# Performance work log

Measured on AMD Instinct MI355X. Metric: run time of the kernel, lower is better.

## Reference

```python
import jax, jax.numpy as jnp
import numpy as np

B, D, T = 8, 1024, 512
HID, NH, NL = 256, 4, 2
OUT = HID // NH  # 64 per-head dim
ALPHA = 0.2      # leaky relu slope
EPS = 1e-5       # layernorm eps


def setup_inputs() -> dict:
    key = jax.random.key(0)
    ks = jax.random.split(key, 10)
    X_obs = jax.random.normal(ks[0], (B, D, T), dtype=jnp.float32)
    mask = (jax.random.uniform(ks[1], (B, D, T)) < 0.8).astype(jnp.float32)
    W_in = jax.random.normal(ks[2], (2 * T, HID), dtype=jnp.float32) * (1.0 / np.sqrt(2 * T))
    b_in = jnp.zeros((HID,), dtype=jnp.float32)
    gat_W = jax.random.normal(ks[3], (NL, NH, HID, OUT), dtype=jnp.float32) * (1.0 / np.sqrt(HID))
    gat_a = jax.random.normal(ks[4], (NL, NH, 2 * OUT), dtype=jnp.float32) * 0.1
    ln_g = jnp.ones((NL, HID), dtype=jnp.float32)
    ln_b = jnp.zeros((NL, HID), dtype=jnp.float32)
    W_out = jax.random.normal(ks[5], (HID, T), dtype=jnp.float32) * (1.0 / np.sqrt(HID))
    b_out = jnp.zeros((T,), dtype=jnp.float32)
    return dict(X_obs=X_obs, mask=mask, W_in=W_in, b_in=b_in, gat_W=gat_W,
                gat_a=gat_a, ln_g=ln_g, ln_b=ln_b, W_out=W_out, b_out=b_out)


def _layer_norm(x, g, b):
    mu = jnp.mean(x, axis=-1, keepdims=True)
    var = jnp.mean((x - mu) ** 2, axis=-1, keepdims=True)
    return (x - mu) * jax.lax.rsqrt(var + EPS) * g + b


def _gat_forward(X_obs, mask, W_in, b_in, gat_W, gat_a, ln_g, ln_b, W_out, b_out):
    # mean-impute per (d, t) position across batch
    obs_sum = jnp.sum(X_obs * mask, axis=0, keepdims=True)
    obs_cnt = jnp.sum(mask, axis=0, keepdims=True)
    pos_mean = obs_sum / (obs_cnt + 1e-10)
    X_mean = X_obs * mask + (1.0 - mask) * pos_mean

    x = jnp.concatenate([X_mean, mask], axis=-1)       # (B, D, 2T)
    h = x @ W_in + b_in                                 # (B, N, HID)

    for l in range(NL):
        Wl = gat_W[l]                                   # (H, HID, OUT)
        a_left = gat_a[l, :, :OUT]                      # (H, OUT)
        a_right = gat_a[l, :, OUT:]                     # (H, OUT)
        hW = jnp.einsum('bnd,hde->bhne', h, Wl)         # (B, H, N, OUT)
        # e_ij = leakyrelu(a_left . h_i + a_right . h_j) -- avoids O(N^2 * 2d) concat
        s_l = jnp.einsum('bhne,he->bhn', hW, a_left)
        s_r = jnp.einsum('bhne,he->bhn', hW, a_right)
        e = jax.nn.leaky_relu(s_l[..., :, None] + s_r[..., None, :], ALPHA)  # (B,H,N,N)
        attn = jax.nn.softmax(e, axis=-1)
        head_out = jnp.einsum('bhnm,bhme->bhne', attn, hW)                   # (B,H,N,OUT)
        h_new = jnp.transpose(head_out, (0, 2, 1, 3)).reshape(h.shape[0], h.shape[1], HID)
        h = _layer_norm(h + h_new, ln_g[l], ln_b[l])

    return h @ W_out + b_out                            # (B, D, T)


def reference(X_obs, mask, W_in, b_in, gat_W, gat_a, ln_g, ln_b, W_out, b_out):
    return _gat_forward(X_obs, mask, W_in, b_in, gat_W, gat_a, ln_g, ln_b, W_out, b_out)
```

## Files before the change

kernel.cpp:

```cpp
#include <hip/hip_runtime.h>
#include <hip/hip_bf16.h>

constexpr int B_   = 8;
constexpr int D_   = 1024;
constexpr int T_   = 512;
constexpr int HID_ = 256;
constexpr int NH_  = 4;
constexpr int NL_  = 2;
constexpr int OUT_ = 64;
constexpr float ALPHA_ = 0.2f;
constexpr float EPS_   = 1e-5f;
constexpr int M_ = B_ * D_;
constexpr int DT_ = D_ * T_;
constexpr int KIN_ = 2 * T_;

typedef __attribute__((ext_vector_type(8))) short short8;
typedef __attribute__((ext_vector_type(4))) float floatx4;

__device__ __forceinline__ unsigned short f2bf(float f) {
    unsigned int u = __float_as_uint(f);
    unsigned int r = u + 0x7fffu + ((u >> 16) & 1u);
    return (unsigned short)(r >> 16);
}
__device__ __forceinline__ float bf2f(unsigned short u) {
    return __uint_as_float((unsigned int)u << 16);
}
__device__ __forceinline__ unsigned int kenc(float f) {
    unsigned int u = __float_as_uint(f);
    return (u & 0x80000000u) ? ~u : (u | 0x80000000u);
}
__device__ __forceinline__ float kdec(unsigned int k) {
    unsigned int u = (k & 0x80000000u) ? (k ^ 0x80000000u) : ~k;
    return __uint_as_float(u);
}

__global__ __launch_bounds__(256) void impute_k(const float* __restrict__ X,
                                                const float* __restrict__ Mk,
                                                unsigned short* __restrict__ Ain) {
    int idx4 = (blockIdx.x * 256 + threadIdx.x) * 4;
    int t = idx4 & (T_ - 1);
    int d = idx4 >> 9;
    float4 x[B_], m[B_];
    float4 s = {0, 0, 0, 0}, c = {0, 0, 0, 0};
#pragma unroll
    for (int b = 0; b < B_; b++) {
        x[b] = *(const float4*)&X[(size_t)b * DT_ + idx4];
        m[b] = *(const float4*)&Mk[(size_t)b * DT_ + idx4];
        s.x += x[b].x * m[b].x; s.y += x[b].y * m[b].y;
        s.z += x[b].z * m[b].z; s.w += x[b].w * m[b].w;
        c.x += m[b].x; c.y += m[b].y; c.z += m[b].z; c.w += m[b].w;
    }
    float4 pm;
    pm.x = s.x / (c.x + 1e-10f); pm.y = s.y / (c.y + 1e-10f);
    pm.z = s.z / (c.z + 1e-10f); pm.w = s.w / (c.w + 1e-10f);
#pragma unroll
    for (int b = 0; b < B_; b++) {
        size_t row = (size_t)b * D_ + d;
        ushort4 xm, mk;
        xm.x = f2bf(x[b].x * m[b].x + (1.f - m[b].x) * pm.x);
        xm.y = f2bf(x[b].y * m[b].y + (1.f - m[b].y) * pm.y);
        xm.z = f2bf(x[b].z * m[b].z + (1.f - m[b].z) * pm.z);
        xm.w = f2bf(x[b].w * m[b].w + (1.f - m[b].w) * pm.w);
        mk.x = f2bf(m[b].x); mk.y = f2bf(m[b].y);
        mk.z = f2bf(m[b].z); mk.w = f2bf(m[b].w);
        *(ushort4*)&Ain[row * KIN_ + t]      = xm;
        *(ushort4*)&Ain[row * KIN_ + T_ + t] = mk;
    }
}

__global__ __launch_bounds__(256) void wprep_k(const float* __restrict__ W_in,
                                               const float* __restrict__ gatW,
                                               const float* __restrict__ W_out,
                                               unsigned short* __restrict__ Wt_in,
                                               unsigned short* __restrict__ Wcat,
                                               unsigned short* __restrict__ WtO,
                                               unsigned int* __restrict__ rmaxkey) {
    int idx = blockIdx.x * 256 + threadIdx.x;
    if (idx < 64) rmaxkey[idx] = 0u;
    if (idx < 262144) {
        int n = idx >> 10, k = idx & 1023;
        Wt_in[idx] = f2bf(W_in[(size_t)k * HID_ + n]);
    } else if (idx < 393216) {
        int j = idx - 262144;
        int l = j >> 16, n = (j >> 8) & 255, k = j & 255;
        int h = n >> 6, e = n & 63;
        Wcat[j] = f2bf(gatW[(((size_t)(l * NH_ + h) * HID_) + k) * OUT_ + e]);
    } else {
        int j = idx - 393216;
        int n = j >> 8, k = j & 255;
        WtO[j] = f2bf(W_out[(size_t)k * T_ + n]);
    }
}

template <int MODE>
__global__ __launch_bounds__(256) void gemm_bf16_k(
        const unsigned short* __restrict__ A,
        const unsigned short* __restrict__ Bt,
        const float* __restrict__ bias,
        float* __restrict__ C,
        unsigned short* __restrict__ Cb,
        const float* __restrict__ ga,
        float* __restrict__ s_l,
        float* __restrict__ s_r,
        unsigned int* __restrict__ rmaxkey,
        int Nsz, int Ksz) {
    __shared__ __align__(16) unsigned short As[2][128 * 32];
    __shared__ __align__(16) unsigned short Bs[2][64 * 32];
    int tid = threadIdx.x;
    int wave = tid >> 6, lane = tid & 63;
    int q = lane >> 4, r16 = lane & 15;
    int rowbase = blockIdx.y * 128;
    int colbase = blockIdx.x * 64;

    int arow0 = tid >> 2,        aoff0 = (tid & 3) * 8;
    int arow1 = (tid + 256) >> 2, aoff1 = (tid & 3) * 8;
    int brow = tid >> 2, boff = (tid & 3) * 8;
    const unsigned short* Ap0 = A + (size_t)(rowbase + arow0) * Ksz + aoff0;
    const unsigned short* Ap1 = A + (size_t)(rowbase + arow1) * Ksz + aoff1;
    const unsigned short* Bp  = Bt + (size_t)(colbase + brow) * Ksz + boff;

    floatx4 acc[2][4];
#pragma unroll
    for (int i = 0; i < 2; i++)
#pragma unroll
        for (int j = 0; j < 4; j++) acc[i][j] = (floatx4)0.f;

    uint4 ar0 = *(const uint4*)Ap0;
    uint4 ar1 = *(const uint4*)Ap1;
    uint4 br  = *(const uint4*)Bp;
    *(uint4*)&As[0][tid * 8]         = ar0;
    *(uint4*)&As[0][(tid + 256) * 8] = ar1;
    *(uint4*)&Bs[0][tid * 8]         = br;

    int nk = Ksz >> 5;
    for (int it = 0; it < nk; it++) {
        int cur = it & 1;
        __syncthreads();
        if (it + 1 < nk) {
            int kt2 = (it + 1) << 5;
            ar0 = *(const uint4*)(Ap0 + kt2);
            ar1 = *(const uint4*)(Ap1 + kt2);
            br  = *(const uint4*)(Bp + kt2);
        }
        short8 a[2], b[4];
#pragma unroll
        for (int mi = 0; mi < 2; mi++)
            a[mi] = *(const short8*)&As[cur][(wave * 32 + mi * 16 + r16) * 32 + q * 8];
#pragma unroll
        for (int ni = 0; ni < 4; ni++)
            b[ni] = *(const short8*)&Bs[cur][(ni * 16 + r16) * 32 + q * 8];
#pragma unroll
        for (int mi = 0; mi < 2; mi++)
#pragma unroll
            for (int ni = 0; ni < 4; ni++)
                acc[mi][ni] = __builtin_amdgcn_mfma_f32_16x16x32_bf16(
                    a[mi], b[ni], acc[mi][ni], 0, 0, 0);
        if (it + 1 < nk) {
            int nxt = cur ^ 1;
            *(uint4*)&As[nxt][tid * 8]         = ar0;
            *(uint4*)&As[nxt][(tid + 256) * 8] = ar1;
            *(uint4*)&Bs[nxt][tid * 8]         = br;
        }
    }
    if constexpr (MODE == 2) {
        int bhh = ((rowbase >> 10) << 2) + blockIdx.x;
        int nbase = (rowbase & (D_ - 1)) + wave * 32;
#pragma unroll
        for (int mi = 0; mi < 2; mi++) {
#pragma unroll
            for (int ni = 0; ni < 4; ni++) {
                int e = ni * 16 + r16;
                ushort4 pk;
                pk.x = f2bf(acc[mi][ni][0]);
                pk.y = f2bf(acc[mi][ni][1]);
                pk.z = f2bf(acc[mi][ni][2]);
                pk.w = f2bf(acc[mi][ni][3]);
                *(ushort4*)&Cb[((size_t)(bhh * 64 + e) << 10) + nbase + mi * 16 + q * 4] = pk;
            }
        }
        const float* gab = ga + blockIdx.x * 2 * OUT_;
        float al4[4], ar4[4];
#pragma unroll
        for (int ni = 0; ni < 4; ni++) {
            al4[ni] = gab[ni * 16 + r16];
            ar4[ni] = gab[OUT_ + ni * 16 + r16];
        }
        float slv[2][4], srv[2][4];
#pragma unroll
        for (int mi = 0; mi < 2; mi++)
#pragma unroll
            for (int rr = 0; rr < 4; rr++) {
                float s1 = 0.f, s2 = 0.f;
#pragma unroll
                for (int ni = 0; ni < 4; ni++) {
                    s1 += acc[mi][ni][rr] * al4[ni];
                    s2 += acc[mi][ni][rr] * ar4[ni];
                }
                slv[mi][rr] = s1;
                srv[mi][rr] = s2;
            }
#pragma unroll
        for (int off = 1; off < 16; off <<= 1) {
#pragma unroll
            for (int mi = 0; mi < 2; mi++)
#pragma unroll
                for (int rr = 0; rr < 4; rr++) {
                    slv[mi][rr] += __shfl_xor(slv[mi][rr], off, 64);
                    srv[mi][rr] += __shfl_xor(srv[mi][rr], off, 64);
                }
        }
        {
            int slot = r16 & 7;
            int mi = slot >> 2, rr = slot & 3;
            int n = nbase + mi * 16 + q * 4 + rr;
            if (r16 < 8) s_l[bhh * D_ + n] = slv[mi][rr];
            else         s_r[bhh * D_ + n] = srv[mi][rr];
        }
        float mx = -1e30f;
#pragma unroll
        for (int mi = 0; mi < 2; mi++)
#pragma unroll
            for (int rr = 0; rr < 4; rr++) mx = fmaxf(mx, srv[mi][rr]);
        if (lane == 0) atomicMax(&rmaxkey[bhh], kenc(mx));
    } else {
#pragma unroll
        for (int mi = 0; mi < 2; mi++) {
#pragma unroll
            for (int rr = 0; rr < 4; rr++) {
                int row = rowbase + wave * 32 + mi * 16 + q * 4 + rr;
#pragma unroll
                for (int ni = 0; ni < 4; ni++) {
                    int col = colbase + ni * 16 + r16;
                    float v = acc[mi][ni][rr] + (bias ? bias[col] : 0.f);
                    C[(size_t)row * Nsz + col] = v;
                    if constexpr (MODE == 1) Cb[(size_t)row * Nsz + col] = f2bf(v);
                }
            }
        }
    }
}

__global__ __launch_bounds__(256) void attn_k(const unsigned short* __restrict__ hwT,
                                              const float* __restrict__ sl_g,
                                              const float* __restrict__ sr_g,
                                              const unsigned int* __restrict__ rmaxkey,
                                              float* __restrict__ hnew) {
    int bh = blockIdx.x;
    int b = bh >> 2, h = bh & 3;
    int tid = threadIdx.x;
    int wave = tid >> 6, lane = tid & 63;
    int q = lane >> 4, r16 = lane & 15;

    __shared__ float srs[D_];
    __shared__ __align__(16) unsigned short Vt[64][136];
    __shared__ float den_lds[64];

    *(float4*)&srs[tid * 4] = *(const float4*)&sr_g[bh * D_ + tid * 4];

    float rm = kdec(rmaxkey[bh]);
    int row0 = blockIdx.y * 64 + wave * 16;
    float sl = sl_g[bh * D_ + row0 + r16];
    float xm = sl + rm;
    float Mn = fmaxf(xm, ALPHA_ * xm);

    floatx4 acc[4];
#pragma unroll
    for (int i = 0; i < 4; i++) acc[i] = (floatx4)0.f;
    float dsum = 0.f;

    const unsigned short* vbase = hwT + ((size_t)(bh * 64) << 10);

    for (int mc = 0; mc < D_; mc += 128) {
        __syncthreads();
#pragma unroll
        for (int i = 0; i < 4; i++) {
            int s = tid + i * 256;
            int e = s >> 4, part = s & 15;
            *(uint4*)&Vt[e][part * 8] = *(const uint4*)&vbase[((size_t)e << 10) + mc + part * 8];
        }
        __syncthreads();
#pragma unroll
        for (int kk = 0; kk < 128; kk += 32) {
            int m0 = mc + kk + q * 8;
            float4 s0 = *(const float4*)&srs[m0];
            float4 s1 = *(const float4*)&srs[m0 + 4];
            float sr8[8] = {s0.x, s0.y, s0.z, s0.w, s1.x, s1.y, s1.z, s1.w};
            float p[8];
#pragma unroll
            for (int j = 0; j < 8; j++) {
                float x = sl + sr8[j];
                float e = fmaxf(x, ALPHA_ * x);
                float pj = __expf(e - Mn);
                dsum += pj;
                p[j] = pj;
            }
            union { unsigned int u[4]; short8 s8; } cv;
#pragma unroll
            for (int j = 0; j < 4; j++) {
                unsigned int lo = (__float_as_uint(p[2 * j]) + 0x8000u) >> 16;
                unsigned int hi = (__float_as_uint(p[2 * j + 1]) + 0x8000u) & 0xffff0000u;
                cv.u[j] = hi | lo;
            }
#pragma unroll
            for (int ni = 0; ni < 4; ni++) {
                short8 bfr = *(const short8*)&Vt[ni * 16 + r16][kk + q * 8];
                acc[ni] = __builtin_amdgcn_mfma_f32_16x16x32_bf16(cv.s8, bfr, acc[ni], 0, 0, 0);
            }
        }
    }
    dsum += __shfl_xor(dsum, 16);
    dsum += __shfl_xor(dsum, 32);
    if (q == 0) den_lds[wave * 16 + r16] = dsum;
    __syncthreads();
#pragma unroll
    for (int rr = 0; rr < 4; rr++) {
        int rloc = q * 4 + rr;
        float rden = 1.f / den_lds[wave * 16 + rloc];
        size_t grow = (size_t)(b * D_ + blockIdx.y * 64 + wave * 16 + rloc);
#pragma unroll
        for (int ni = 0; ni < 4; ni++) {
            hnew[grow * HID_ + h * OUT_ + ni * 16 + r16] = acc[ni][rr] * rden;
        }
    }
}

__global__ __launch_bounds__(256) void addln_k(float* __restrict__ h,
                                               const float* __restrict__ hn,
                                               const float* __restrict__ g,
                                               const float* __restrict__ bb,
                                               unsigned short* __restrict__ hbf) {
    int wave = threadIdx.x >> 6, lane = threadIdx.x & 63;
    size_t row = (size_t)blockIdx.x * 4 + wave;
    float4 a = *(const float4*)&h[row * HID_ + lane * 4];
    float4 r = *(const float4*)&hn[row * HID_ + lane * 4];
    float4 v = {a.x + r.x, a.y + r.y, a.z + r.z, a.w + r.w};
    float s = v.x + v.y + v.z + v.w;
#pragma unroll
    for (int off = 1; off < 64; off <<= 1) s += __shfl_xor(s, off, 64);
    float mu = s * (1.f / HID_);
    float4 d = {v.x - mu, v.y - mu, v.z - mu, v.w - mu};
    float s2 = d.x * d.x + d.y * d.y + d.z * d.z + d.w * d.w;
#pragma unroll
    for (int off = 1; off < 64; off <<= 1) s2 += __shfl_xor(s2, off, 64);
    float rs = rsqrtf(s2 * (1.f / HID_) + EPS_);
    float4 gg = *(const float4*)&g[lane * 4];
    float4 bbv = *(const float4*)&bb[lane * 4];
    float4 res;
    res.x = d.x * rs * gg.x + bbv.x;
    res.y = d.y * rs * gg.y + bbv.y;
    res.z = d.z * rs * gg.z + bbv.z;
    res.w = d.w * rs * gg.w + bbv.w;
    *(float4*)&h[row * HID_ + lane * 4] = res;
    ushort4 pk = {f2bf(res.x), f2bf(res.y), f2bf(res.z), f2bf(res.w)};
    *(ushort4*)&hbf[row * HID_ + lane * 4] = pk;
}

extern "C" void kernel_launch(void* const* d_in, const int* in_sizes, int n_in,
                              void* d_out, int out_size, void* d_ws, size_t ws_size,
                              hipStream_t stream) {
    const float* X_obs = (const float*)d_in[0];
    const float* mask  = (const float*)d_in[1];
    const float* W_in  = (const float*)d_in[2];
    const float* b_in  = (const float*)d_in[3];
    const float* gat_W = (const float*)d_in[4];
    const float* gat_a = (const float*)d_in[5];
    const float* ln_g  = (const float*)d_in[6];
    const float* ln_b  = (const float*)d_in[7];
    const float* W_out = (const float*)d_in[8];
    const float* b_out = (const float*)d_in[9];
    float* out = (float*)d_out;

    char* base = (char*)d_ws;
    unsigned short* Ain  = (unsigned short*)base;
    unsigned short* hwT  = (unsigned short*)base;
    float* hnew = (float*)(base + (4u << 20));
    float* hbuf = (float*)(base + (16u << 20));
    unsigned short* hbf   = (unsigned short*)(base + (24u << 20));
    unsigned short* Wt_in = (unsigned short*)(base + (28u << 20));
    unsigned short* Wcat  = Wt_in + (size_t)HID_ * KIN_;
    unsigned short* WtO   = Wcat + (size_t)NL_ * HID_ * HID_;
    float* slb = (float*)(WtO + (size_t)T_ * HID_);
    float* srb = slb + B_ * NH_ * D_;
    unsigned int* rmaxkey = (unsigned int*)(srb + B_ * NH_ * D_);

    impute_k<<<DT_ / 1024, 256, 0, stream>>>(X_obs, mask, Ain);
    wprep_k<<<2048, 256, 0, stream>>>(W_in, gat_W, W_out, Wt_in, Wcat, WtO, rmaxkey);

    gemm_bf16_k<1><<<dim3(HID_ / 64, M_ / 128), 256, 0, stream>>>(
        Ain, Wt_in, b_in, hbuf, hbf, nullptr, nullptr, nullptr, nullptr,
        HID_, KIN_);

    for (int l = 0; l < NL_; l++) {
        gemm_bf16_k<2><<<dim3(HID_ / 64, M_ / 128), 256, 0, stream>>>(
            hbf, Wcat + (size_t)l * HID_ * HID_, nullptr, nullptr, hwT,
            gat_a + (size_t)l * NH_ * 2 * OUT_, slb, srb, rmaxkey + l * 32,
            HID_, HID_);
        attn_k<<<dim3(B_ * NH_, D_ / 64), 256, 0, stream>>>(
            hwT, slb, srb, rmaxkey + l * 32, hnew);
        addln_k<<<M_ / 4, 256, 0, stream>>>(hbuf, hnew, ln_g + (size_t)l * HID_,
                                            ln_b + (size_t)l * HID_, hbf);
    }

    gemm_bf16_k<0><<<dim3(T_ / 64, M_ / 128), 256, 0, stream>>>(
        hbf, WtO, b_out, out, nullptr, nullptr, nullptr, nullptr, nullptr,
        T_, HID_);
}
```

Measured before the change: 223.3 us.

## Use direct global-to-LDS loads in GEMM and double-buffer V tiles in attention

The GEMM kernel now stages A and B tiles with global_load_lds, writing straight into shared memory instead of through registers, which drops the register round-trip and the separate LDS stores. The attention kernel now double-buffers the V tile and prefetches the next 128-column chunk into registers while MFMAs run on the current one, which removes one barrier per chunk and hides global latency. One risk in the GEMM path is that the async LDS loads are consumed after __syncthreads with no explicit vmcnt wait, so correctness depends on compiler-inserted waits. The added buffer also raises LDS and register use in attention.

```diff
diff --git a/kernel.cpp b/kernel.cpp
--- a/kernel.cpp
+++ b/kernel.cpp
@@ -7,9 +7,9 @@
 constexpr int HID_ = 256;
 constexpr int NH_  = 4;
 constexpr int NL_  = 2;
-constexpr int OUT_ = 64;
 constexpr float ALPHA_ = 0.2f;
 constexpr float EPS_   = 1e-5f;
+constexpr int OUT_ = 64;
 constexpr int M_ = B_ * D_;
 constexpr int DT_ = D_ * T_;
 constexpr int KIN_ = 2 * T_;
@@ -32,6 +32,11 @@
 __device__ __forceinline__ float kdec(unsigned int k) {
     unsigned int u = (k & 0x80000000u) ? (k ^ 0x80000000u) : ~k;
     return __uint_as_float(u);
+}
+__device__ __forceinline__ void gll16(const unsigned short* g, unsigned short* l) {
+    __builtin_amdgcn_global_load_lds(
+        (const __attribute__((address_space(1))) void*)g,
+        (__attribute__((address_space(3))) void*)l, 16, 0, 0);
 }
 
 __global__ __launch_bounds__(256) void impute_k(const float* __restrict__ X,
@@ -112,12 +117,9 @@
     int rowbase = blockIdx.y * 128;
     int colbase = blockIdx.x * 64;
 
-    int arow0 = tid >> 2,        aoff0 = (tid & 3) * 8;
-    int arow1 = (tid + 256) >> 2, aoff1 = (tid & 3) * 8;
-    int brow = tid >> 2, boff = (tid & 3) * 8;
-    const unsigned short* Ap0 = A + (size_t)(rowbase + arow0) * Ksz + aoff0;
-    const unsigned short* Ap1 = A + (size_t)(rowbase + arow1) * Ksz + aoff1;
-    const unsigned short* Bp  = Bt + (size_t)(colbase + brow) * Ksz + boff;
+    const unsigned short* Ap0 = A + (size_t)(rowbase + (tid >> 2)) * Ksz + (tid & 3) * 8;
+    const unsigned short* Ap1 = A + (size_t)(rowbase + (tid >> 2) + 64) * Ksz + (tid & 3) * 8;
+    const unsigned short* Bp  = Bt + (size_t)(colbase + (tid >> 2)) * Ksz + (tid & 3) * 8;
 
     floatx4 acc[2][4];
 #pragma unroll
@@ -125,12 +127,9 @@
 #pragma unroll
         for (int j = 0; j < 4; j++) acc[i][j] = (floatx4)0.f;
 
-    uint4 ar0 = *(const uint4*)Ap0;
-    uint4 ar1 = *(const uint4*)Ap1;
-    uint4 br  = *(const uint4*)Bp;
-    *(uint4*)&As[0][tid * 8]         = ar0;
-    *(uint4*)&As[0][(tid + 256) * 8] = ar1;
-    *(uint4*)&Bs[0][tid * 8]         = br;
+    gll16(Ap0, &As[0][tid * 8]);
+    gll16(Ap1, &As[0][(tid + 256) * 8]);
+    gll16(Bp,  &Bs[0][tid * 8]);
 
     int nk = Ksz >> 5;
     for (int it = 0; it < nk; it++) {
@@ -138,9 +137,9 @@
         __syncthreads();
         if (it + 1 < nk) {
             int kt2 = (it + 1) << 5;
-            ar0 = *(const uint4*)(Ap0 + kt2);
-            ar1 = *(const uint4*)(Ap1 + kt2);
-            br  = *(const uint4*)(Bp + kt2);
+            gll16(Ap0 + kt2, &As[cur ^ 1][tid * 8]);
+            gll16(Ap1 + kt2, &As[cur ^ 1][(tid + 256) * 8]);
+            gll16(Bp + kt2,  &Bs[cur ^ 1][tid * 8]);
         }
         short8 a[2], b[4];
 #pragma unroll
@@ -155,12 +154,6 @@
             for (int ni = 0; ni < 4; ni++)
                 acc[mi][ni] = __builtin_amdgcn_mfma_f32_16x16x32_bf16(
                     a[mi], b[ni], acc[mi][ni], 0, 0, 0);
-        if (it + 1 < nk) {
-            int nxt = cur ^ 1;
-            *(uint4*)&As[nxt][tid * 8]         = ar0;
-            *(uint4*)&As[nxt][(tid + 256) * 8] = ar1;
-            *(uint4*)&Bs[nxt][tid * 8]         = br;
-        }
     }
     if constexpr (MODE == 2) {
         int bhh = ((rowbase >> 10) << 2) + blockIdx.x;
@@ -252,7 +245,7 @@
     int q = lane >> 4, r16 = lane & 15;
 
     __shared__ float srs[D_];
-    __shared__ __align__(16) unsigned short Vt[64][136];
+    __shared__ __align__(16) unsigned short Vt[2][64][136];
     __shared__ float den_lds[64];
 
     *(float4*)&srs[tid * 4] = *(const float4*)&sr_g[bh * D_ + tid * 4];
@@ -269,19 +262,34 @@
     float dsum = 0.f;
 
     const unsigned short* vbase = hwT + ((size_t)(bh * 64) << 10);
-
-    for (int mc = 0; mc < D_; mc += 128) {
-        __syncthreads();
-#pragma unroll
-        for (int i = 0; i < 4; i++) {
-            int s = tid + i * 256;
-            int e = s >> 4, part = s & 15;
-            *(uint4*)&Vt[e][part * 8] = *(const uint4*)&vbase[((size_t)e << 10) + mc + part * 8];
-        }
-        __syncthreads();
+    int se[4], sp[4];
+#pragma unroll
+    for (int i = 0; i < 4; i++) {
+        int s = tid + i * 256;
+        se[i] = s >> 4;
+        sp[i] = (s & 15) * 8;
+    }
+
+    uint4 pre[4];
+#pragma unroll
+    for (int i = 0; i < 4; i++)
+        pre[i] = *(const uint4*)&vbase[((size_t)se[i] << 10) + sp[i]];
+#pragma unroll
+    for (int i = 0; i < 4; i++)
+        *(uint4*)&Vt[0][se[i]][sp[i]] = pre[i];
+    __syncthreads();
+
+    for (int c = 0; c < 8; c++) {
+        int cur = c & 1;
+        if (c < 7) {
+            int mc = (c + 1) * 128;
+#pragma unroll
+            for (int i = 0; i < 4; i++)
+                pre[i] = *(const uint4*)&vbase[((size_t)se[i] << 10) + mc + sp[i]];
+        }
 #pragma unroll
         for (int kk = 0; kk < 128; kk += 32) {
-            int m0 = mc + kk + q * 8;
+            int m0 = c * 128 + kk + q * 8;
             float4 s0 = *(const float4*)&srs[m0];
             float4 s1 = *(const float4*)&srs[m0 + 4];
             float sr8[8] = {s0.x, s0.y, s0.z, s0.w, s1.x, s1.y, s1.z, s1.w};
@@ -303,10 +311,16 @@
             }
 #pragma unroll
             for (int ni = 0; ni < 4; ni++) {
-                short8 bfr = *(const short8*)&Vt[ni * 16 + r16][kk + q * 8];
+                short8 bfr = *(const short8*)&Vt[cur][ni * 16 + r16][kk + q * 8];
                 acc[ni] = __builtin_amdgcn_mfma_f32_16x16x32_bf16(cv.s8, bfr, acc[ni], 0, 0, 0);
             }
         }
+        if (c < 7) {
+#pragma unroll
+            for (int i = 0; i < 4; i++)
+                *(uint4*)&Vt[cur ^ 1][se[i]][sp[i]] = pre[i];
+        }
+        __syncthreads();
     }
     dsum += __shfl_xor(dsum, 16);
     dsum += __shfl_xor(dsum, 32);
```

Result: no change. 224.9 us (+0.7%).
